# Performance work log

Hardware: AMD Instinct MI355X
Metric: run time of the kernel (lower is better)

## Reference

```python
import jax, jax.numpy as jnp
import numpy as np

NEG = -1000000000.0

def setup_inputs() -> dict:
    key = jax.random.key(0)
    kq, kk, kv, km = jax.random.split(key, 4)
    B, H, S, D = 2, 4, 4096, 64
    q = jax.random.normal(kq, (B, H, S, D), dtype=jnp.float32)
    k = jax.random.normal(kk, (B, H, S, D), dtype=jnp.float32)
    v = jax.random.normal(kv, (B, H, S, D), dtype=jnp.float32)
    mask = jax.random.randint(km, (1, S, S), 0, 2, dtype=jnp.int32)
    return {"q": q, "k": k, "v": v, "mask": mask}

def reference(q, k, v, mask):
    # scores: [B,H,S,S]
    attn = jnp.einsum('bhsd,bhtd->bhst', q, k)
    attn = attn / jnp.sqrt(jnp.asarray(k.shape[-1], dtype=jnp.float32))
    # torch cat/view just broadcasts mask [1,S,S] to [B,H,S,S]
    m = jnp.broadcast_to(mask.astype(bool)[:, None, :, :], attn.shape)
    attn = jnp.where(m, jnp.float32(NEG), attn)
    # NOTE: original module uses nn.Softmax(dim=0) -> softmax over batch axis
    attn = jax.nn.softmax(attn, axis=0)
    out = jnp.einsum('bhst,bhtd->bhsd', attn, v)
    return (out, attn)
```

## Files before the change

kernel.cpp:

```cpp
#include <hip/hip_runtime.h>

#define SDIM 4096
#define DDIM 64
#define HDIM 4
#define OUTN (2 * HDIM * SDIM * DDIM)

typedef short short8 __attribute__((ext_vector_type(8)));
typedef short bh4    __attribute__((ext_vector_type(4)));
typedef float f32x4  __attribute__((ext_vector_type(4)));

__device__ inline short f2bf(float f) {
    unsigned u = __builtin_bit_cast(unsigned, f);
    u = (u + 0x7fffu + ((u >> 16) & 1u)) >> 16;
    return (short)u;
}
__device__ inline float bf2f(short s) {
    unsigned u = ((unsigned)(unsigned short)s) << 16;
    return __builtin_bit_cast(float, u);
}

__device__ inline short* ldsp(short* base, int row, int colshort) {
    int byte = (row << 7) + (colshort << 1);
    byte ^= (row & 7) << 4;
    return (short*)((char*)base + byte);
}

__device__ inline void g2l16(const short* g, short* l) {
    __builtin_amdgcn_global_load_lds(
        (const __attribute__((address_space(1))) unsigned int*)g,
        (__attribute__((address_space(3))) unsigned int*)l, 16, 0, 0);
}

__global__ void pack_mask(const int* __restrict__ mask,
                          unsigned long long* __restrict__ bits) {
    int gid = blockIdx.x * 256 + threadIdx.x;
    int v = (mask[gid] != 0);
    unsigned long long bal = __ballot(v);
    if ((threadIdx.x & 63) == 0) bits[gid >> 6] = bal;
}

__global__ void cvt_bf16(const float* __restrict__ src, short* __restrict__ dst) {
    int gid = blockIdx.x * 256 + threadIdx.x;
    const float* p = src + (size_t)gid * 8;
    f32x4 a = *(const f32x4*)p;
    f32x4 b = *(const f32x4*)(p + 4);
    short8 o;
#pragma unroll
    for (int j = 0; j < 4; ++j) { o[j] = f2bf(a[j]); o[j + 4] = f2bf(b[j]); }
    *(short8*)(dst + (size_t)gid * 8) = o;
}

__global__ void transpose_v(const float* __restrict__ v, short* __restrict__ vt) {
    int gid = blockIdx.x * 256 + threadIdx.x;
    int t8 = gid & (SDIM / 8 - 1);
    int d  = (gid >> 9) & (DDIM - 1);
    int bh = gid >> 15;
    short8 o;
#pragma unroll
    for (int j = 0; j < 8; ++j)
        o[j] = f2bf(v[((size_t)bh * SDIM + t8 * 8 + j) * DDIM + d]);
    *(short8*)(vt + ((size_t)bh * DDIM + d) * SDIM + t8 * 8) = o;
}

__global__ __launch_bounds__(256, 2)
void attn_fused(const short* __restrict__ qg, const short* __restrict__ kg,
                const short* __restrict__ vtg,
                const unsigned long long* __restrict__ mbits,
                float* __restrict__ attng, float* __restrict__ opart) {
    __shared__ short Ks [2][64 * 64];
    __shared__ short VTs[2][64 * 64];
    __shared__ short Ps [2][64 * 64];

    const int h   = blockIdx.y;
    const int s0  = blockIdx.x << 6;
    const int tz  = blockIdx.z;
    const int tid = threadIdx.x;
    const int wv  = tid >> 6;
    const int ln  = tid & 63;
    const int l   = ln & 15;
    const int qd  = ln >> 4;

    short8 qf[2][2];
#pragma unroll
    for (int b = 0; b < 2; ++b) {
        const size_t rb = ((size_t)(b * HDIM + h) * SDIM + (s0 + wv * 16 + l)) * DDIM;
#pragma unroll
        for (int kc = 0; kc < 2; ++kc)
            qf[b][kc] = *(const short8*)(qg + rb + kc * 32 + qd * 8);
    }

    f32x4 oacc[2][4];
#pragma unroll
    for (int b = 0; b < 2; ++b)
#pragma unroll
        for (int nd = 0; nd < 4; ++nd)
            oacc[b][nd] = (f32x4){0.f, 0.f, 0.f, 0.f};

    const int ln8 = ln >> 3;
    const int sc_ = (ln & 7) ^ ln8;
    const int mrow0 = s0 + wv * 16 + qd * 4;

    const int tbeg = tz * (SDIM / 2);
    for (int t0 = tbeg; t0 < tbeg + SDIM / 2; t0 += 64) {
        __syncthreads();
#pragma unroll
        for (int b = 0; b < 2; ++b) {
            const short* kb = kg  + ((size_t)(b * HDIM + h) * SDIM + t0) * DDIM;
            const short* vb = vtg + ((size_t)(b * HDIM + h) * DDIM) * SDIM + t0;
#pragma unroll
            for (int p = 0; p < 2; ++p) {
                int rr = p * 32 + wv * 8 + ln8;
                g2l16(kb + (size_t)rr * DDIM + sc_ * 8, &Ks [b][p * 2048 + wv * 512]);
                g2l16(vb + (size_t)rr * SDIM + sc_ * 8, &VTs[b][p * 2048 + wv * 512]);
            }
        }
        unsigned long long mw[4];
#pragma unroll
        for (int rg = 0; rg < 4; ++rg)
            mw[rg] = mbits[(size_t)(mrow0 + rg) * (SDIM / 64) + (t0 >> 6)];
        __syncthreads();

        f32x4 sc[2][4];
#pragma unroll
        for (int b = 0; b < 2; ++b)
#pragma unroll
            for (int nt = 0; nt < 4; ++nt) {
                f32x4 acc = (f32x4){0.f, 0.f, 0.f, 0.f};
#pragma unroll
                for (int kc = 0; kc < 2; ++kc) {
                    short8 bf = *(const short8*)ldsp(&Ks[b][0], nt * 16 + l, kc * 32 + qd * 8);
                    acc = __builtin_amdgcn_mfma_f32_16x16x32_bf16(qf[b][kc], bf, acc, 0, 0, 0);
                }
                sc[b][nt] = acc;
            }

#pragma unroll
        for (int nt = 0; nt < 4; ++nt)
#pragma unroll
            for (int rg = 0; rg < 4; ++rg) {
                float dd = (sc[0][nt][rg] - sc[1][nt][rg]) * 0.125f;
                bool msk = (mw[rg] >> (nt * 16 + l)) & 1ull;
                float p0 = msk ? 0.5f : __builtin_amdgcn_rcpf(1.f + __expf(-dd));
                float p1 = 1.f - p0;
                int row = wv * 16 + qd * 4 + rg;
                *ldsp(&Ps[0][0], row, nt * 16 + l) = f2bf(p0);
                *ldsp(&Ps[1][0], row, nt * 16 + l) = f2bf(p1);
            }

#pragma unroll
        for (int b = 0; b < 2; ++b)
#pragma unroll
            for (int kc = 0; kc < 2; ++kc) {
                short8 af = *(const short8*)ldsp(&Ps[b][0], wv * 16 + l, kc * 32 + qd * 8);
#pragma unroll
                for (int nd = 0; nd < 4; ++nd) {
                    short8 bf = *(const short8*)ldsp(&VTs[b][0], nd * 16 + l, kc * 32 + qd * 8);
                    oacc[b][nd] = __builtin_amdgcn_mfma_f32_16x16x32_bf16(af, bf, oacc[b][nd], 0, 0, 0);
                }
            }

        {
            int rr2 = ln >> 4;
            int c2  = ln & 15;
#pragma unroll
            for (int b = 0; b < 2; ++b) {
                size_t ab = ((size_t)(b * HDIM + h) * SDIM + s0) * (size_t)SDIM + t0;
#pragma unroll
                for (int sub = 0; sub < 4; ++sub) {
                    int row = wv * 16 + sub * 4 + rr2;
                    bh4 pv = *(const bh4*)ldsp(&Ps[b][0], row, c2 * 4);
                    f32x4 o;
#pragma unroll
                    for (int j = 0; j < 4; ++j) o[j] = bf2f(pv[j]);
                    __builtin_nontemporal_store(
                        o, (f32x4*)(attng + ab + (size_t)row * SDIM + c2 * 4));
                }
            }
        }
    }

#pragma unroll
    for (int b = 0; b < 2; ++b)
#pragma unroll
        for (int nd = 0; nd < 4; ++nd)
#pragma unroll
            for (int rg = 0; rg < 4; ++rg) {
                int srow = s0 + wv * 16 + qd * 4 + rg;
                opart[(size_t)tz * OUTN +
                      ((size_t)(b * HDIM + h) * SDIM + srow) * DDIM + nd * 16 + l] =
                    oacc[b][nd][rg];
            }
}

__global__ void combine(const float* __restrict__ opart, float* __restrict__ outg) {
    int gid = blockIdx.x * 256 + threadIdx.x;
    f32x4 a = *(const f32x4*)(opart + (size_t)gid * 4);
    f32x4 b = *(const f32x4*)(opart + (size_t)OUTN + (size_t)gid * 4);
    *(f32x4*)(outg + (size_t)gid * 4) = a + b;
}

extern "C" void kernel_launch(void* const* d_in, const int* in_sizes, int n_in,
                              void* d_out, int out_size, void* d_ws, size_t ws_size,
                              hipStream_t stream) {
    (void)in_sizes; (void)n_in; (void)out_size; (void)ws_size;
    const float* qg  = (const float*)d_in[0];
    const float* kg  = (const float*)d_in[1];
    const float* vg  = (const float*)d_in[2];
    const int*   msk = (const int*)d_in[3];

    float* outg  = (float*)d_out;
    float* attng = outg + (size_t)OUTN;

    char* ws = (char*)d_ws;
    unsigned long long* bits = (unsigned long long*)ws;
    short* qb = (short*)(ws + (size_t) 2 * 1024 * 1024);
    short* kb = (short*)(ws + (size_t) 6 * 1024 * 1024);
    short* vt = (short*)(ws + (size_t)10 * 1024 * 1024);
    float* op = (float*)(ws + (size_t)14 * 1024 * 1024);

    pack_mask  <<<dim3(SDIM * SDIM / 256), dim3(256), 0, stream>>>(msk, bits);
    cvt_bf16   <<<dim3(OUTN / (8 * 256)), dim3(256), 0, stream>>>(qg, qb);
    cvt_bf16   <<<dim3(OUTN / (8 * 256)), dim3(256), 0, stream>>>(kg, kb);
    transpose_v<<<dim3(OUTN / (8 * 256)), dim3(256), 0, stream>>>(vg, vt);
    attn_fused <<<dim3(SDIM / 64, HDIM, 2), dim3(256), 0, stream>>>(qb, kb, vt, bits, attng, op);
    combine    <<<dim3(OUTN / (4 * 256)), dim3(256), 0, stream>>>(op, outg);
}
```

Before: 210.6 us.

## Split key range four ways, share one P tile, derive second batch as 1-p

Raises the key-dimension split from 2 to 4 so the grid has more blocks. The first split writes its partial output straight into the output buffer, and combine sums the other three partials into it. The second batch's probability tile is no longer stored in LDS; it is recomputed as 1-p from the first, which halves the P shared-memory footprint. Launch bounds rise to 3 blocks per SM to raise occupancy. The cost is more partial-output traffic in combine and extra conversion work in the inner loop.

```diff
diff --git a/kernel.cpp b/kernel.cpp
--- a/kernel.cpp
+++ b/kernel.cpp
@@ -4,6 +4,7 @@
 #define DDIM 64
 #define HDIM 4
 #define OUTN (2 * HDIM * SDIM * DDIM)
+#define NTZ 4
 
 typedef short short8 __attribute__((ext_vector_type(8)));
 typedef short bh4    __attribute__((ext_vector_type(4)));
@@ -62,14 +63,15 @@
     *(short8*)(vt + ((size_t)bh * DDIM + d) * SDIM + t8 * 8) = o;
 }
 
-__global__ __launch_bounds__(256, 2)
+__global__ __launch_bounds__(256, 3)
 void attn_fused(const short* __restrict__ qg, const short* __restrict__ kg,
                 const short* __restrict__ vtg,
                 const unsigned long long* __restrict__ mbits,
-                float* __restrict__ attng, float* __restrict__ opart) {
+                float* __restrict__ attng, float* __restrict__ outg,
+                float* __restrict__ opart) {
     __shared__ short Ks [2][64 * 64];
     __shared__ short VTs[2][64 * 64];
-    __shared__ short Ps [2][64 * 64];
+    __shared__ short Ps [64 * 64];
 
     const int h   = blockIdx.y;
     const int s0  = blockIdx.x << 6;
@@ -100,8 +102,8 @@
     const int sc_ = (ln & 7) ^ ln8;
     const int mrow0 = s0 + wv * 16 + qd * 4;
 
-    const int tbeg = tz * (SDIM / 2);
-    for (int t0 = tbeg; t0 < tbeg + SDIM / 2; t0 += 64) {
+    const int tbeg = tz * (SDIM / NTZ);
+    for (int t0 = tbeg; t0 < tbeg + SDIM / NTZ; t0 += 64) {
         __syncthreads();
 #pragma unroll
         for (int b = 0; b < 2; ++b) {
@@ -141,44 +143,46 @@
                 float dd = (sc[0][nt][rg] - sc[1][nt][rg]) * 0.125f;
                 bool msk = (mw[rg] >> (nt * 16 + l)) & 1ull;
                 float p0 = msk ? 0.5f : __builtin_amdgcn_rcpf(1.f + __expf(-dd));
-                float p1 = 1.f - p0;
                 int row = wv * 16 + qd * 4 + rg;
-                *ldsp(&Ps[0][0], row, nt * 16 + l) = f2bf(p0);
-                *ldsp(&Ps[1][0], row, nt * 16 + l) = f2bf(p1);
-            }
-
-#pragma unroll
-        for (int b = 0; b < 2; ++b)
-#pragma unroll
-            for (int kc = 0; kc < 2; ++kc) {
-                short8 af = *(const short8*)ldsp(&Ps[b][0], wv * 16 + l, kc * 32 + qd * 8);
-#pragma unroll
-                for (int nd = 0; nd < 4; ++nd) {
-                    short8 bf = *(const short8*)ldsp(&VTs[b][0], nd * 16 + l, kc * 32 + qd * 8);
-                    oacc[b][nd] = __builtin_amdgcn_mfma_f32_16x16x32_bf16(af, bf, oacc[b][nd], 0, 0, 0);
-                }
-            }
+                *ldsp(&Ps[0], row, nt * 16 + l) = f2bf(p0);
+            }
+
+#pragma unroll
+        for (int kc = 0; kc < 2; ++kc) {
+            short8 af0 = *(const short8*)ldsp(&Ps[0], wv * 16 + l, kc * 32 + qd * 8);
+            short8 af1;
+#pragma unroll
+            for (int j = 0; j < 8; ++j) af1[j] = f2bf(1.f - bf2f(af0[j]));
+#pragma unroll
+            for (int nd = 0; nd < 4; ++nd) {
+                short8 bf = *(const short8*)ldsp(&VTs[0][0], nd * 16 + l, kc * 32 + qd * 8);
+                oacc[0][nd] = __builtin_amdgcn_mfma_f32_16x16x32_bf16(af0, bf, oacc[0][nd], 0, 0, 0);
+                short8 bf1 = *(const short8*)ldsp(&VTs[1][0], nd * 16 + l, kc * 32 + qd * 8);
+                oacc[1][nd] = __builtin_amdgcn_mfma_f32_16x16x32_bf16(af1, bf1, oacc[1][nd], 0, 0, 0);
+            }
+        }
 
         {
             int rr2 = ln >> 4;
             int c2  = ln & 15;
-#pragma unroll
-            for (int b = 0; b < 2; ++b) {
-                size_t ab = ((size_t)(b * HDIM + h) * SDIM + s0) * (size_t)SDIM + t0;
-#pragma unroll
-                for (int sub = 0; sub < 4; ++sub) {
-                    int row = wv * 16 + sub * 4 + rr2;
-                    bh4 pv = *(const bh4*)ldsp(&Ps[b][0], row, c2 * 4);
-                    f32x4 o;
-#pragma unroll
-                    for (int j = 0; j < 4; ++j) o[j] = bf2f(pv[j]);
-                    __builtin_nontemporal_store(
-                        o, (f32x4*)(attng + ab + (size_t)row * SDIM + c2 * 4));
-                }
+            size_t ab0 = ((size_t)(0 * HDIM + h) * SDIM + s0) * (size_t)SDIM + t0;
+            size_t ab1 = ((size_t)(1 * HDIM + h) * SDIM + s0) * (size_t)SDIM + t0;
+#pragma unroll
+            for (int sub = 0; sub < 4; ++sub) {
+                int row = wv * 16 + sub * 4 + rr2;
+                bh4 pv = *(const bh4*)ldsp(&Ps[0], row, c2 * 4);
+                f32x4 o0, o1;
+#pragma unroll
+                for (int j = 0; j < 4; ++j) { o0[j] = bf2f(pv[j]); o1[j] = 1.f - o0[j]; }
+                __builtin_nontemporal_store(
+                    o0, (f32x4*)(attng + ab0 + (size_t)row * SDIM + c2 * 4));
+                __builtin_nontemporal_store(
+                    o1, (f32x4*)(attng + ab1 + (size_t)row * SDIM + c2 * 4));
             }
         }
     }
 
+    float* dst = (tz == 0) ? outg : (opart + (size_t)(tz - 1) * OUTN);
 #pragma unroll
     for (int b = 0; b < 2; ++b)
 #pragma unroll
@@ -186,17 +190,18 @@
 #pragma unroll
             for (int rg = 0; rg < 4; ++rg) {
                 int srow = s0 + wv * 16 + qd * 4 + rg;
-                opart[(size_t)tz * OUTN +
-                      ((size_t)(b * HDIM + h) * SDIM + srow) * DDIM + nd * 16 + l] =
+                dst[((size_t)(b * HDIM + h) * SDIM + srow) * DDIM + nd * 16 + l] =
                     oacc[b][nd][rg];
             }
 }
 
 __global__ void combine(const float* __restrict__ opart, float* __restrict__ outg) {
     int gid = blockIdx.x * 256 + threadIdx.x;
-    f32x4 a = *(const f32x4*)(opart + (size_t)gid * 4);
-    f32x4 b = *(const f32x4*)(opart + (size_t)OUTN + (size_t)gid * 4);
-    *(f32x4*)(outg + (size_t)gid * 4) = a + b;
+    f32x4 a = *(const f32x4*)(outg + (size_t)gid * 4);
+#pragma unroll
+    for (int s = 0; s < NTZ - 1; ++s)
+        a = a + *(const f32x4*)(opart + (size_t)s * OUTN + (size_t)gid * 4);
+    *(f32x4*)(outg + (size_t)gid * 4) = a;
 }
 
 extern "C" void kernel_launch(void* const* d_in, const int* in_sizes, int n_in,
@@ -222,6 +227,7 @@
     cvt_bf16   <<<dim3(OUTN / (8 * 256)), dim3(256), 0, stream>>>(qg, qb);
     cvt_bf16   <<<dim3(OUTN / (8 * 256)), dim3(256), 0, stream>>>(kg, kb);
     transpose_v<<<dim3(OUTN / (8 * 256)), dim3(256), 0, stream>>>(vg, vt);
-    attn_fused <<<dim3(SDIM / 64, HDIM, 2), dim3(256), 0, stream>>>(qb, kb, vt, bits, attng, op);
+    attn_fused <<<dim3(SDIM / 64, HDIM, NTZ), dim3(256), 0, stream>>>(
+        qb, kb, vt, bits, attng, outg, op);
     combine    <<<dim3(OUTN / (4 * 256)), dim3(256), 0, stream>>>(op, outg);
 }
```

Result: slower. 217.9 us (+3.5%).

## Store only p0 in LDS and batch attention writes over four key tiles

Applied to the files above, without the earlier changes.

The probability tile in LDS now holds only p0 across four consecutive 64-wide key tiles (a 64x256 buffer). The p1 = 1-p0 operand is derived in registers for the PV MFMA instead of being stored. The attention-matrix writeback happens once every four tiles, so each row writes 256 contiguous floats per burst, which should give longer global write streams and fewer LDS writes. It costs extra register arithmetic for the 1-p conversion. p1 is now rounded from bf16 p0 rather than computed in fp32, so it may differ slightly in the last bits.

```diff
diff --git a/kernel.cpp b/kernel.cpp
--- a/kernel.cpp
+++ b/kernel.cpp
@@ -21,6 +21,12 @@
 
 __device__ inline short* ldsp(short* base, int row, int colshort) {
     int byte = (row << 7) + (colshort << 1);
+    byte ^= (row & 7) << 4;
+    return (short*)((char*)base + byte);
+}
+
+__device__ inline short* ldsp2(short* base, int row, int colshort) {
+    int byte = (row << 9) + (colshort << 1);
     byte ^= (row & 7) << 4;
     return (short*)((char*)base + byte);
 }
@@ -69,7 +75,7 @@
                 float* __restrict__ attng, float* __restrict__ opart) {
     __shared__ short Ks [2][64 * 64];
     __shared__ short VTs[2][64 * 64];
-    __shared__ short Ps [2][64 * 64];
+    __shared__ short Ps [64 * 256];
 
     const int h   = blockIdx.y;
     const int s0  = blockIdx.x << 6;
@@ -120,6 +126,8 @@
             mw[rg] = mbits[(size_t)(mrow0 + rg) * (SDIM / 64) + (t0 >> 6)];
         __syncthreads();
 
+        const int g = (t0 >> 6) & 3;
+
         f32x4 sc[2][4];
 #pragma unroll
         for (int b = 0; b < 2; ++b)
@@ -141,39 +149,48 @@
                 float dd = (sc[0][nt][rg] - sc[1][nt][rg]) * 0.125f;
                 bool msk = (mw[rg] >> (nt * 16 + l)) & 1ull;
                 float p0 = msk ? 0.5f : __builtin_amdgcn_rcpf(1.f + __expf(-dd));
-                float p1 = 1.f - p0;
                 int row = wv * 16 + qd * 4 + rg;
-                *ldsp(&Ps[0][0], row, nt * 16 + l) = f2bf(p0);
-                *ldsp(&Ps[1][0], row, nt * 16 + l) = f2bf(p1);
-            }
-
-#pragma unroll
-        for (int b = 0; b < 2; ++b)
-#pragma unroll
-            for (int kc = 0; kc < 2; ++kc) {
-                short8 af = *(const short8*)ldsp(&Ps[b][0], wv * 16 + l, kc * 32 + qd * 8);
-#pragma unroll
-                for (int nd = 0; nd < 4; ++nd) {
-                    short8 bf = *(const short8*)ldsp(&VTs[b][0], nd * 16 + l, kc * 32 + qd * 8);
-                    oacc[b][nd] = __builtin_amdgcn_mfma_f32_16x16x32_bf16(af, bf, oacc[b][nd], 0, 0, 0);
-                }
-            }
-
-        {
+                *ldsp2(&Ps[0], row, g * 64 + nt * 16 + l) = f2bf(p0);
+            }
+
+#pragma unroll
+        for (int kc = 0; kc < 2; ++kc) {
+            short8 af0 = *(const short8*)ldsp2(&Ps[0], wv * 16 + l, g * 64 + kc * 32 + qd * 8);
+            short8 af1;
+#pragma unroll
+            for (int j = 0; j < 8; ++j) af1[j] = f2bf(1.f - bf2f(af0[j]));
+#pragma unroll
+            for (int nd = 0; nd < 4; ++nd) {
+                short8 bf0 = *(const short8*)ldsp(&VTs[0][0], nd * 16 + l, kc * 32 + qd * 8);
+                oacc[0][nd] = __builtin_amdgcn_mfma_f32_16x16x32_bf16(af0, bf0, oacc[0][nd], 0, 0, 0);
+                short8 bf1 = *(const short8*)ldsp(&VTs[1][0], nd * 16 + l, kc * 32 + qd * 8);
+                oacc[1][nd] = __builtin_amdgcn_mfma_f32_16x16x32_bf16(af1, bf1, oacc[1][nd], 0, 0, 0);
+            }
+        }
+
+        if (g == 3) {
             int rr2 = ln >> 4;
             int c2  = ln & 15;
+            int tg0 = t0 & ~255;
 #pragma unroll
             for (int b = 0; b < 2; ++b) {
-                size_t ab = ((size_t)(b * HDIM + h) * SDIM + s0) * (size_t)SDIM + t0;
+                size_t ab = ((size_t)(b * HDIM + h) * SDIM + s0) * (size_t)SDIM + tg0;
 #pragma unroll
                 for (int sub = 0; sub < 4; ++sub) {
                     int row = wv * 16 + sub * 4 + rr2;
-                    bh4 pv = *(const bh4*)ldsp(&Ps[b][0], row, c2 * 4);
-                    f32x4 o;
-#pragma unroll
-                    for (int j = 0; j < 4; ++j) o[j] = bf2f(pv[j]);
-                    __builtin_nontemporal_store(
-                        o, (f32x4*)(attng + ab + (size_t)row * SDIM + c2 * 4));
+                    float* dst = attng + ab + (size_t)row * SDIM;
+#pragma unroll
+                    for (int tch = 0; tch < 4; ++tch) {
+                        bh4 pv = *(const bh4*)ldsp2(&Ps[0], row, tch * 64 + c2 * 4);
+                        f32x4 o;
+#pragma unroll
+                        for (int j = 0; j < 4; ++j) {
+                            float v = bf2f(pv[j]);
+                            o[j] = b ? 1.f - v : v;
+                        }
+                        __builtin_nontemporal_store(
+                            o, (f32x4*)(dst + tch * 64 + c2 * 4));
+                    }
                 }
             }
         }
```

Measured after the change: 208.4 us. About the same (-1.0%).
